# Kernel optimization log

Measured on AMD Instinct MI355X. Metric: run time of the kernel, lower is better.

## Reference

```python
import jax, jax.numpy as jnp
import numpy as np

N_NODES = 100000
N_EDGES = 1250000
HIDDEN = 64


def setup_inputs() -> dict:
    key = jax.random.key(0)
    ks = jax.random.split(key, 8)
    x = jax.random.normal(ks[0], (N_NODES, HIDDEN), dtype=jnp.float32)
    edge_index = jax.random.randint(ks[1], (2, N_EDGES), 0, N_NODES, dtype=jnp.int64)
    s = 1.0 / np.sqrt(HIDDEN)
    # PyG SAGEConv params: lin_l (neighbor path, with bias), lin_r (root path, no bias)
    W1l = jax.random.uniform(ks[2], (HIDDEN, HIDDEN), jnp.float32, -s, s)
    b1l = jnp.zeros((HIDDEN,), jnp.float32)
    W1r = jax.random.uniform(ks[3], (HIDDEN, HIDDEN), jnp.float32, -s, s)
    W2l = jax.random.uniform(ks[4], (HIDDEN, HIDDEN), jnp.float32, -s, s)
    b2l = jnp.zeros((HIDDEN,), jnp.float32)
    W2r = jax.random.uniform(ks[5], (HIDDEN, HIDDEN), jnp.float32, -s, s)
    return {"x": x, "edge_index": edge_index, "W1l": W1l, "b1l": b1l,
            "W1r": W1r, "W2l": W2l, "b2l": b2l, "W2r": W2r}


def _sage_conv(x, src, dst, Wl, bl, Wr, num_nodes):
    # mean-aggregate neighbor (source) features at target nodes
    agg = jax.ops.segment_sum(x[src], dst, num_segments=num_nodes)  # [N, H]
    cnt = jax.ops.segment_sum(jnp.ones((src.shape[0],), x.dtype), dst,
                              num_segments=num_nodes)               # [N]
    mean = agg / jnp.maximum(cnt, 1.0)[:, None]
    # out = lin_l(mean_neighbors) + lin_r(x_root)
    return mean @ Wl + bl + x @ Wr


def reference(x, edge_index, W1l, b1l, W1r, W2l, b2l, W2r):
    src, dst = edge_index[0], edge_index[1]
    n = x.shape[0]
    h = jax.nn.relu(_sage_conv(x, src, dst, W1l, b1l, W1r, n))
    return _sage_conv(h, src, dst, W2l, b2l, W2r, n)
```

## Files before the change

kernel.cpp:

```cpp
#include <hip/hip_runtime.h>
#include <hip/hip_bf16.h>

#define HIDDEN 64
#define TN 64
#define APAD 132

__global__ __launch_bounds__(256) void k_hist(
    const int* __restrict__ ei, int* __restrict__ deg, int nEdges)
{
    for (int e = blockIdx.x * blockDim.x + threadIdx.x; e < nEdges;
         e += gridDim.x * blockDim.x) {
        atomicAdd(&deg[ei[nEdges + e]], 1);
    }
}

__global__ __launch_bounds__(1024) void k_scan(
    const int* __restrict__ deg, int* __restrict__ rowPtr,
    int* __restrict__ cursor, int n)
{
    __shared__ int part[1024];
    const int t = threadIdx.x;
    const int seg = (n + 1023) / 1024;
    const int beg = t * seg;
    const int end = min(beg + seg, n);
    int s = 0;
    for (int i = beg; i < end; ++i) s += deg[i];
    part[t] = s;
    __syncthreads();
    for (int off = 1; off < 1024; off <<= 1) {
        int v = (t >= off) ? part[t - off] : 0;
        __syncthreads();
        part[t] += v;
        __syncthreads();
    }
    int run = (t == 0) ? 0 : part[t - 1];
    for (int i = beg; i < end; ++i) {
        const int d = deg[i];
        rowPtr[i] = run;
        cursor[i] = run;
        run += d;
    }
    if (beg < n && end == n) rowPtr[n] = run;
}

__global__ __launch_bounds__(256) void k_fill(
    const int* __restrict__ ei, int* __restrict__ cursor,
    int* __restrict__ csrSrc, int nEdges)
{
    for (int e = blockIdx.x * blockDim.x + threadIdx.x; e < nEdges;
         e += gridDim.x * blockDim.x) {
        const int dst = ei[nEdges + e];
        const int pos = atomicAdd(&cursor[dst], 1);
        csrSrc[pos] = ei[e];
    }
}

__device__ __forceinline__ void gemm_pass(
    const float (*sA)[APAD], const float (*sB)[HIDDEN],
    int tr, int tc, int kOff, float acc[4][4])
{
#pragma unroll
    for (int k4 = 0; k4 < 16; ++k4) {
        float A_[4][4], B_[4][4];
#pragma unroll
        for (int r = 0; r < 4; ++r) {
            const float4 t4 = *(const float4*)&sA[tr * 4 + r][kOff + k4 * 4];
            A_[r][0] = t4.x; A_[r][1] = t4.y; A_[r][2] = t4.z; A_[r][3] = t4.w;
        }
#pragma unroll
        for (int kk = 0; kk < 4; ++kk) {
            const float4 t4 = *(const float4*)&sB[k4 * 4 + kk][tc * 4];
            B_[kk][0] = t4.x; B_[kk][1] = t4.y; B_[kk][2] = t4.z; B_[kk][3] = t4.w;
        }
#pragma unroll
        for (int kk = 0; kk < 4; ++kk)
#pragma unroll
            for (int r = 0; r < 4; ++r)
#pragma unroll
                for (int j = 0; j < 4; ++j)
                    acc[r][j] = fmaf(A_[r][kk], B_[kk][j], acc[r][j]);
    }
}

template <bool RELU>
__global__ __launch_bounds__(256) void k_fused(
    const float* __restrict__ xin,
    const int* __restrict__ rowPtr,
    const int* __restrict__ csrSrc,
    const float* __restrict__ Wl,
    const float* __restrict__ bl,
    const float* __restrict__ Wr,
    float* __restrict__ outp,
    int nNodes)
{
    __shared__ __align__(16) float sA[TN][APAD];
    __shared__ __align__(16) float sB[HIDDEN][HIDDEN];

    const int w    = threadIdx.x >> 6;
    const int lane = threadIdx.x & 63;
    const int tr   = threadIdx.x >> 4;
    const int tc   = threadIdx.x & 15;

    for (int i = threadIdx.x; i < HIDDEN * HIDDEN; i += 256)
        sB[i >> 6][i & 63] = Wl[i];

    float bias[4];
#pragma unroll
    for (int jj = 0; jj < 4; ++jj) bias[jj] = bl[tc * 4 + jj];

    const int base = blockIdx.x * TN;

    for (int n = w * 16; n < w * 16 + 16; ++n) {
        const int g = base + n;
        if (g < nNodes) {
            const int beg = rowPtr[g], end = rowPtr[g + 1];
            float acc0 = 0.f, acc1 = 0.f;
            int i = beg;
            for (; i + 7 < end; i += 8) {
                const int s0 = csrSrc[i + 0], s1 = csrSrc[i + 1];
                const int s2 = csrSrc[i + 2], s3 = csrSrc[i + 3];
                const int s4 = csrSrc[i + 4], s5 = csrSrc[i + 5];
                const int s6 = csrSrc[i + 6], s7 = csrSrc[i + 7];
                acc0 += xin[s0 * HIDDEN + lane] + xin[s1 * HIDDEN + lane]
                      + xin[s2 * HIDDEN + lane] + xin[s3 * HIDDEN + lane];
                acc1 += xin[s4 * HIDDEN + lane] + xin[s5 * HIDDEN + lane]
                      + xin[s6 * HIDDEN + lane] + xin[s7 * HIDDEN + lane];
            }
            for (; i < end; ++i) acc0 += xin[csrSrc[i] * HIDDEN + lane];
            acc0 += acc1;
            const float inv = (end > beg) ? 1.0f / (float)(end - beg) : 1.0f;
            sA[n][lane]      = acc0 * inv;
            sA[n][64 + lane] = xin[g * HIDDEN + lane];
        } else {
            sA[n][lane]      = 0.f;
            sA[n][64 + lane] = 0.f;
        }
    }
    __syncthreads();

    float acc[4][4];
#pragma unroll
    for (int r = 0; r < 4; ++r)
#pragma unroll
        for (int jj = 0; jj < 4; ++jj) acc[r][jj] = bias[jj];
    gemm_pass(sA, sB, tr, tc, 0, acc);

    __syncthreads();
    for (int i = threadIdx.x; i < HIDDEN * HIDDEN; i += 256)
        sB[i >> 6][i & 63] = Wr[i];
    __syncthreads();

    gemm_pass(sA, sB, tr, tc, 64, acc);

#pragma unroll
    for (int r = 0; r < 4; ++r) {
        const int g = base + tr * 4 + r;
        if (g < nNodes) {
            float4 o;
            o.x = acc[r][0]; o.y = acc[r][1]; o.z = acc[r][2]; o.w = acc[r][3];
            if (RELU) {
                o.x = fmaxf(o.x, 0.f); o.y = fmaxf(o.y, 0.f);
                o.z = fmaxf(o.z, 0.f); o.w = fmaxf(o.w, 0.f);
            }
            *(float4*)&outp[g * HIDDEN + tc * 4] = o;
        }
    }
}

extern "C" void kernel_launch(void* const* d_in, const int* in_sizes, int n_in,
                              void* d_out, int out_size, void* d_ws, size_t ws_size,
                              hipStream_t stream)
{
    const float* x   = (const float*)d_in[0];
    const int*   ei  = (const int*)d_in[1];
    const float* W1l = (const float*)d_in[2];
    const float* b1l = (const float*)d_in[3];
    const float* W1r = (const float*)d_in[4];
    const float* W2l = (const float*)d_in[5];
    const float* b2l = (const float*)d_in[6];
    const float* W2r = (const float*)d_in[7];
    float* out = (float*)d_out;

    const int nNodes = in_sizes[0] / HIDDEN;
    const int nEdges = in_sizes[1] / 2;

    float* h      = (float*)d_ws;
    int*   deg    = (int*)(h + (size_t)nNodes * HIDDEN);
    int*   rowPtr = deg + (nNodes + 1);
    int*   cursor = rowPtr + (nNodes + 1);
    int*   csrSrc = cursor + nNodes;

    const int nTiles = (nNodes + TN - 1) / TN;

    hipMemsetAsync(deg, 0, (size_t)(nNodes + 1) * sizeof(int), stream);
    k_hist<<<2048, 256, 0, stream>>>(ei, deg, nEdges);
    k_scan<<<1, 1024, 0, stream>>>(deg, rowPtr, cursor, nNodes);
    k_fill<<<2048, 256, 0, stream>>>(ei, cursor, csrSrc, nEdges);

    k_fused<true><<<nTiles, 256, 0, stream>>>(x, rowPtr, csrSrc, W1l, b1l, W1r,
                                              h, nNodes);
    k_fused<false><<<nTiles, 256, 0, stream>>>(h, rowPtr, csrSrc, W2l, b2l, W2r,
                                               out, nNodes);
}
```

Before: 1.223 ms.

## Split fused SAGE layer into separate gather-mean and GEMM kernels

Replaces the fused per-tile kernel, where each wave gathered 16 nodes serially under a large shared-memory footprint, with two kernels. The first is a lightweight aggregation kernel that assigns one wave per node with a high occupancy hint. The second is a GEMM kernel that loads precomputed means and root features with float4 loads. The goal is to hide gather latency with many more waves in flight. The cost is an extra round trip of the mean tensor through global memory, with the output buffer reused as scratch, including an in-place read/write in the second layer's GEMM.

```diff
diff --git a/kernel.cpp b/kernel.cpp
--- a/kernel.cpp
+++ b/kernel.cpp
@@ -3,7 +3,7 @@
 
 #define HIDDEN 64
 #define TN 64
-#define APAD 132
+#define APAD 68
 
 __global__ __launch_bounds__(256) void k_hist(
     const int* __restrict__ ei, int* __restrict__ deg, int nEdges)
@@ -55,16 +55,53 @@
     }
 }
 
+__global__ __launch_bounds__(256, 8) void k_agg(
+    const float* __restrict__ xin,
+    const int* __restrict__ rowPtr,
+    const int* __restrict__ csrSrc,
+    float* __restrict__ mean,
+    int nNodes)
+{
+    const int node = blockIdx.x * 4 + (threadIdx.x >> 6);
+    const int lane = threadIdx.x & 63;
+    if (node >= nNodes) return;
+    const int beg = rowPtr[node], end = rowPtr[node + 1];
+    float a0 = 0.f, a1 = 0.f;
+    int i = beg;
+#pragma unroll 1
+    for (; i + 7 < end; i += 8) {
+        const int s0 = csrSrc[i + 0], s1 = csrSrc[i + 1];
+        const int s2 = csrSrc[i + 2], s3 = csrSrc[i + 3];
+        const int s4 = csrSrc[i + 4], s5 = csrSrc[i + 5];
+        const int s6 = csrSrc[i + 6], s7 = csrSrc[i + 7];
+        a0 += xin[s0 * HIDDEN + lane] + xin[s1 * HIDDEN + lane]
+            + xin[s2 * HIDDEN + lane] + xin[s3 * HIDDEN + lane];
+        a1 += xin[s4 * HIDDEN + lane] + xin[s5 * HIDDEN + lane]
+            + xin[s6 * HIDDEN + lane] + xin[s7 * HIDDEN + lane];
+    }
+#pragma unroll 1
+    for (; i + 3 < end; i += 4) {
+        const int s0 = csrSrc[i + 0], s1 = csrSrc[i + 1];
+        const int s2 = csrSrc[i + 2], s3 = csrSrc[i + 3];
+        a0 += xin[s0 * HIDDEN + lane] + xin[s1 * HIDDEN + lane];
+        a1 += xin[s2 * HIDDEN + lane] + xin[s3 * HIDDEN + lane];
+    }
+#pragma unroll 1
+    for (; i < end; ++i) a0 += xin[csrSrc[i] * HIDDEN + lane];
+    const float inv = (end > beg) ? 1.0f / (float)(end - beg) : 1.0f;
+    mean[node * HIDDEN + lane] = (a0 + a1) * inv;
+}
+
 __device__ __forceinline__ void gemm_pass(
     const float (*sA)[APAD], const float (*sB)[HIDDEN],
-    int tr, int tc, int kOff, float acc[4][4])
+    int tr, int tc, float acc[4][4])
 {
 #pragma unroll
     for (int k4 = 0; k4 < 16; ++k4) {
         float A_[4][4], B_[4][4];
 #pragma unroll
         for (int r = 0; r < 4; ++r) {
-            const float4 t4 = *(const float4*)&sA[tr * 4 + r][kOff + k4 * 4];
+            const float4 t4 = *(const float4*)&sA[tr * 4 + r][k4 * 4];
             A_[r][0] = t4.x; A_[r][1] = t4.y; A_[r][2] = t4.z; A_[r][3] = t4.w;
         }
 #pragma unroll
@@ -83,74 +120,59 @@
 }
 
 template <bool RELU>
-__global__ __launch_bounds__(256) void k_fused(
+__global__ __launch_bounds__(256, 3) void k_gemm(
+    const float* __restrict__ mean,
     const float* __restrict__ xin,
-    const int* __restrict__ rowPtr,
-    const int* __restrict__ csrSrc,
     const float* __restrict__ Wl,
     const float* __restrict__ bl,
     const float* __restrict__ Wr,
     float* __restrict__ outp,
     int nNodes)
 {
-    __shared__ __align__(16) float sA[TN][APAD];
+    __shared__ __align__(16) float sM[TN][APAD];
+    __shared__ __align__(16) float sX[TN][APAD];
     __shared__ __align__(16) float sB[HIDDEN][HIDDEN];
 
-    const int w    = threadIdx.x >> 6;
-    const int lane = threadIdx.x & 63;
-    const int tr   = threadIdx.x >> 4;
-    const int tc   = threadIdx.x & 15;
+    const int tr = threadIdx.x >> 4;
+    const int tc = threadIdx.x & 15;
+    const int base = blockIdx.x * TN;
 
     for (int i = threadIdx.x; i < HIDDEN * HIDDEN; i += 256)
         sB[i >> 6][i & 63] = Wl[i];
 
+    for (int idx = threadIdx.x; idx < TN * 16; idx += 256) {
+        const int row = idx >> 4, c4 = idx & 15;
+        const int g = base + row;
+        float4 m4 = make_float4(0.f, 0.f, 0.f, 0.f);
+        float4 x4 = make_float4(0.f, 0.f, 0.f, 0.f);
+        if (g < nNodes) {
+            m4 = *(const float4*)&mean[g * HIDDEN + c4 * 4];
+            x4 = *(const float4*)&xin[g * HIDDEN + c4 * 4];
+        }
+        *(float4*)&sM[row][c4 * 4] = m4;
+        *(float4*)&sX[row][c4 * 4] = x4;
+    }
+
     float bias[4];
 #pragma unroll
-    for (int jj = 0; jj < 4; ++jj) bias[jj] = bl[tc * 4 + jj];
-
-    const int base = blockIdx.x * TN;
-
-    for (int n = w * 16; n < w * 16 + 16; ++n) {
-        const int g = base + n;
-        if (g < nNodes) {
-            const int beg = rowPtr[g], end = rowPtr[g + 1];
-            float acc0 = 0.f, acc1 = 0.f;
-            int i = beg;
-            for (; i + 7 < end; i += 8) {
-                const int s0 = csrSrc[i + 0], s1 = csrSrc[i + 1];
-                const int s2 = csrSrc[i + 2], s3 = csrSrc[i + 3];
-                const int s4 = csrSrc[i + 4], s5 = csrSrc[i + 5];
-                const int s6 = csrSrc[i + 6], s7 = csrSrc[i + 7];
-                acc0 += xin[s0 * HIDDEN + lane] + xin[s1 * HIDDEN + lane]
-                      + xin[s2 * HIDDEN + lane] + xin[s3 * HIDDEN + lane];
-                acc1 += xin[s4 * HIDDEN + lane] + xin[s5 * HIDDEN + lane]
-                      + xin[s6 * HIDDEN + lane] + xin[s7 * HIDDEN + lane];
-            }
-            for (; i < end; ++i) acc0 += xin[csrSrc[i] * HIDDEN + lane];
-            acc0 += acc1;
-            const float inv = (end > beg) ? 1.0f / (float)(end - beg) : 1.0f;
-            sA[n][lane]      = acc0 * inv;
-            sA[n][64 + lane] = xin[g * HIDDEN + lane];
-        } else {
-            sA[n][lane]      = 0.f;
-            sA[n][64 + lane] = 0.f;
-        }
-    }
+    for (int j = 0; j < 4; ++j) bias[j] = bl[tc * 4 + j];
+
     __syncthreads();
 
     float acc[4][4];
 #pragma unroll
     for (int r = 0; r < 4; ++r)
 #pragma unroll
-        for (int jj = 0; jj < 4; ++jj) acc[r][jj] = bias[jj];
-    gemm_pass(sA, sB, tr, tc, 0, acc);
+        for (int j = 0; j < 4; ++j) acc[r][j] = bias[j];
+
+    gemm_pass(sM, sB, tr, tc, acc);
 
     __syncthreads();
     for (int i = threadIdx.x; i < HIDDEN * HIDDEN; i += 256)
         sB[i >> 6][i & 63] = Wr[i];
     __syncthreads();
 
-    gemm_pass(sA, sB, tr, tc, 64, acc);
+    gemm_pass(sX, sB, tr, tc, acc);
 
 #pragma unroll
     for (int r = 0; r < 4; ++r) {
@@ -191,14 +213,16 @@
     int*   csrSrc = cursor + nNodes;
 
     const int nTiles = (nNodes + TN - 1) / TN;
+    const int aggGrid = (nNodes + 3) / 4;
 
     hipMemsetAsync(deg, 0, (size_t)(nNodes + 1) * sizeof(int), stream);
     k_hist<<<2048, 256, 0, stream>>>(ei, deg, nEdges);
     k_scan<<<1, 1024, 0, stream>>>(deg, rowPtr, cursor, nNodes);
     k_fill<<<2048, 256, 0, stream>>>(ei, cursor, csrSrc, nEdges);
 
-    k_fused<true><<<nTiles, 256, 0, stream>>>(x, rowPtr, csrSrc, W1l, b1l, W1r,
-                                              h, nNodes);
-    k_fused<false><<<nTiles, 256, 0, stream>>>(h, rowPtr, csrSrc, W2l, b2l, W2r,
-                                               out, nNodes);
-}
+    k_agg<<<aggGrid, 256, 0, stream>>>(x, rowPtr, csrSrc, out, nNodes);
+    k_gemm<true><<<nTiles, 256, 0, stream>>>(out, x, W1l, b1l, W1r, h, nNodes);
+
+    k_agg<<<aggGrid, 256, 0, stream>>>(h, rowPtr, csrSrc, out, nNodes);
+    k_gemm<false><<<nTiles, 256, 0, stream>>>(out, h, W2l, b2l, W2r, out, nNodes);
+}
```

Measured after the change: 1.334 ms. 9.0% more time.

## Parallelize CSR prefix scan across blocks and mask-unroll neighbor gather

Applied to the files above, without the earlier changes.

Replaces the single-block serial-segment scan with a three-kernel multi-block scan (per-chunk scan, block-sum scan, offset add) so the rowPtr construction runs across many CUs. The neighbor gather loop is rewritten to process eight edges per iteration with clamped indices and multiplicative masks, removing the scalar tail loop. It also adds a launch-bounds occupancy hint of three blocks per CU. In exchange it adds two extra kernel launches and performs wasted masked loads on the final partial group of each row.

```diff
diff --git a/kernel.cpp b/kernel.cpp
--- a/kernel.cpp
+++ b/kernel.cpp
@@ -14,33 +14,56 @@
     }
 }
 
-__global__ __launch_bounds__(1024) void k_scan(
+__global__ __launch_bounds__(256) void k_scan1(
     const int* __restrict__ deg, int* __restrict__ rowPtr,
-    int* __restrict__ cursor, int n)
-{
-    __shared__ int part[1024];
+    int* __restrict__ blockSum, int n)
+{
+    __shared__ int tmp[256];
     const int t = threadIdx.x;
-    const int seg = (n + 1023) / 1024;
-    const int beg = t * seg;
-    const int end = min(beg + seg, n);
-    int s = 0;
-    for (int i = beg; i < end; ++i) s += deg[i];
-    part[t] = s;
-    __syncthreads();
-    for (int off = 1; off < 1024; off <<= 1) {
-        int v = (t >= off) ? part[t - off] : 0;
-        __syncthreads();
-        part[t] += v;
-        __syncthreads();
-    }
-    int run = (t == 0) ? 0 : part[t - 1];
-    for (int i = beg; i < end; ++i) {
-        const int d = deg[i];
-        rowPtr[i] = run;
-        cursor[i] = run;
-        run += d;
-    }
-    if (beg < n && end == n) rowPtr[n] = run;
+    const int i = blockIdx.x * 256 + t;
+    const int v = (i < n) ? deg[i] : 0;
+    tmp[t] = v;
+    __syncthreads();
+#pragma unroll
+    for (int off = 1; off < 256; off <<= 1) {
+        const int u = (t >= off) ? tmp[t - off] : 0;
+        __syncthreads();
+        tmp[t] += u;
+        __syncthreads();
+    }
+    if (i < n) rowPtr[i] = tmp[t] - v;
+    if (t == 255) blockSum[blockIdx.x] = tmp[255];
+}
+
+__global__ __launch_bounds__(512) void k_scan2(
+    int* __restrict__ blockSum, int* __restrict__ rowPtr, int nb, int n)
+{
+    __shared__ int tmp[512];
+    const int t = threadIdx.x;
+    const int v = (t < nb) ? blockSum[t] : 0;
+    tmp[t] = v;
+    __syncthreads();
+#pragma unroll
+    for (int off = 1; off < 512; off <<= 1) {
+        const int u = (t >= off) ? tmp[t - off] : 0;
+        __syncthreads();
+        tmp[t] += u;
+        __syncthreads();
+    }
+    if (t < nb) blockSum[t] = tmp[t] - v;
+    if (t == nb - 1) rowPtr[n] = tmp[t];
+}
+
+__global__ __launch_bounds__(256) void k_scan3(
+    int* __restrict__ rowPtr, int* __restrict__ cursor,
+    const int* __restrict__ blockSum, int n)
+{
+    const int i = blockIdx.x * 256 + threadIdx.x;
+    if (i < n) {
+        const int v = rowPtr[i] + blockSum[blockIdx.x];
+        rowPtr[i] = v;
+        cursor[i] = v;
+    }
 }
 
 __global__ __launch_bounds__(256) void k_fill(
@@ -83,7 +106,7 @@
 }
 
 template <bool RELU>
-__global__ __launch_bounds__(256) void k_fused(
+__global__ __launch_bounds__(256, 3) void k_fused(
     const float* __restrict__ xin,
     const int* __restrict__ rowPtr,
     const int* __restrict__ csrSrc,
@@ -100,41 +123,38 @@
     const int lane = threadIdx.x & 63;
     const int tr   = threadIdx.x >> 4;
     const int tc   = threadIdx.x & 15;
+    const int base = blockIdx.x * TN;
 
     for (int i = threadIdx.x; i < HIDDEN * HIDDEN; i += 256)
         sB[i >> 6][i & 63] = Wl[i];
 
-    float bias[4];
-#pragma unroll
-    for (int jj = 0; jj < 4; ++jj) bias[jj] = bl[tc * 4 + jj];
-
-    const int base = blockIdx.x * TN;
-
+#pragma unroll 1
     for (int n = w * 16; n < w * 16 + 16; ++n) {
         const int g = base + n;
+        float a0 = 0.f, a1 = 0.f, root = 0.f, inv = 1.f;
         if (g < nNodes) {
             const int beg = rowPtr[g], end = rowPtr[g + 1];
-            float acc0 = 0.f, acc1 = 0.f;
-            int i = beg;
-            for (; i + 7 < end; i += 8) {
-                const int s0 = csrSrc[i + 0], s1 = csrSrc[i + 1];
-                const int s2 = csrSrc[i + 2], s3 = csrSrc[i + 3];
-                const int s4 = csrSrc[i + 4], s5 = csrSrc[i + 5];
-                const int s6 = csrSrc[i + 6], s7 = csrSrc[i + 7];
-                acc0 += xin[s0 * HIDDEN + lane] + xin[s1 * HIDDEN + lane]
-                      + xin[s2 * HIDDEN + lane] + xin[s3 * HIDDEN + lane];
-                acc1 += xin[s4 * HIDDEN + lane] + xin[s5 * HIDDEN + lane]
-                      + xin[s6 * HIDDEN + lane] + xin[s7 * HIDDEN + lane];
+            if (end > beg) {
+                const int last = end - 1;
+#pragma unroll 1
+                for (int i = beg; i < end; i += 8) {
+#pragma unroll
+                    for (int k = 0; k < 8; k += 2) {
+                        const int iA = i + k, iB = i + k + 1;
+                        const int sA_ = csrSrc[min(iA, last)];
+                        const int sB_ = csrSrc[min(iB, last)];
+                        const float mA = (iA < end) ? 1.f : 0.f;
+                        const float mB = (iB < end) ? 1.f : 0.f;
+                        a0 = fmaf(mA, xin[sA_ * HIDDEN + lane], a0);
+                        a1 = fmaf(mB, xin[sB_ * HIDDEN + lane], a1);
+                    }
+                }
+                inv = 1.0f / (float)(end - beg);
             }
-            for (; i < end; ++i) acc0 += xin[csrSrc[i] * HIDDEN + lane];
-            acc0 += acc1;
-            const float inv = (end > beg) ? 1.0f / (float)(end - beg) : 1.0f;
-            sA[n][lane]      = acc0 * inv;
-            sA[n][64 + lane] = xin[g * HIDDEN + lane];
-        } else {
-            sA[n][lane]      = 0.f;
-            sA[n][64 + lane] = 0.f;
-        }
+            root = xin[g * HIDDEN + lane];
+        }
+        sA[n][lane]      = (a0 + a1) * inv;
+        sA[n][64 + lane] = root;
     }
     __syncthreads();
 
@@ -142,7 +162,7 @@
 #pragma unroll
     for (int r = 0; r < 4; ++r)
 #pragma unroll
-        for (int jj = 0; jj < 4; ++jj) acc[r][jj] = bias[jj];
+        for (int j = 0; j < 4; ++j) acc[r][j] = bl[tc * 4 + j];
     gemm_pass(sA, sB, tr, tc, 0, acc);
 
     __syncthreads();
@@ -184,17 +204,21 @@
     const int nNodes = in_sizes[0] / HIDDEN;
     const int nEdges = in_sizes[1] / 2;
 
-    float* h      = (float*)d_ws;
-    int*   deg    = (int*)(h + (size_t)nNodes * HIDDEN);
-    int*   rowPtr = deg + (nNodes + 1);
-    int*   cursor = rowPtr + (nNodes + 1);
-    int*   csrSrc = cursor + nNodes;
-
-    const int nTiles = (nNodes + TN - 1) / TN;
+    float* h        = (float*)d_ws;
+    int*   deg      = (int*)(h + (size_t)nNodes * HIDDEN);
+    int*   rowPtr   = deg + (nNodes + 1);
+    int*   cursor   = rowPtr + (nNodes + 1);
+    int*   csrSrc   = cursor + nNodes;
+    int*   blockSum = csrSrc + nEdges;
+
+    const int nTiles  = (nNodes + TN - 1) / TN;
+    const int nChunks = (nNodes + 255) / 256;
 
     hipMemsetAsync(deg, 0, (size_t)(nNodes + 1) * sizeof(int), stream);
     k_hist<<<2048, 256, 0, stream>>>(ei, deg, nEdges);
-    k_scan<<<1, 1024, 0, stream>>>(deg, rowPtr, cursor, nNodes);
+    k_scan1<<<nChunks, 256, 0, stream>>>(deg, rowPtr, blockSum, nNodes);
+    k_scan2<<<1, 512, 0, stream>>>(blockSum, rowPtr, nChunks, nNodes);
+    k_scan3<<<nChunks, 256, 0, stream>>>(rowPtr, cursor, blockSum, nNodes);
     k_fill<<<2048, 256, 0, stream>>>(ei, cursor, csrSrc, nEdges);
 
     k_fused<true><<<nTiles, 256, 0, stream>>>(x, rowPtr, csrSrc, W1l, b1l, W1r,
```

New measurement: 1.192 ms. 1.03x faster.
